# Optimization experiments

Hardware: AMD Instinct MI355X
Metric: run time of the kernel (lower is better)

## Reference

```python
import jax, jax.numpy as jnp
import numpy as np
from jax import lax

B, H, W = 8, 500, 500
M = 2048          # per-image cap on active bottleneck voxels (ragged -> fixed)
GRID = 125        # bottleneck grid size
ENC_RANGE = 125.0
HEADS, ATTN_CH, CH = 4, 128, 64
EPS = 1e-5
NEG = -1e9

def _conv(x, w, b, stride, pad):
    y = lax.conv_general_dilated(x, w, (stride, stride), pad,
                                 dimension_numbers=('NCHW', 'HWIO', 'NCHW'))
    return y + b[None, :, None, None]

def _maxpool2(m):
    return lax.reduce_window(m, -jnp.inf, lax.max, (1, 1, 2, 2), (1, 1, 2, 2), 'VALID')

def setup_inputs():
    key = jax.random.key(0)
    ks = jax.random.split(key, 12)
    occ = (jax.random.uniform(ks[0], (B, 1, H, W)) < 0.005).astype(jnp.float32)
    x = jax.random.normal(ks[1], (B, 1, H, W), dtype=jnp.float32) * occ
    def rn(k, shape, scale):
        return jax.random.normal(k, shape, dtype=jnp.float32) * scale
    return {
        'x': x,
        'w0': rn(ks[2], (3, 3, 1, 32), 0.3), 'b0': jnp.zeros(32, jnp.float32),
        'g0': jnp.ones(32, jnp.float32), 'be0': jnp.zeros(32, jnp.float32),
        'w1': rn(ks[3], (2, 2, 32, 64), 0.1), 'b1': jnp.zeros(64, jnp.float32),
        'g1': jnp.ones(64, jnp.float32), 'be1': jnp.zeros(64, jnp.float32),
        'w2': rn(ks[4], (2, 2, 64, 64), 0.08), 'b2': jnp.zeros(64, jnp.float32),
        'g2': jnp.ones(64, jnp.float32), 'be2': jnp.zeros(64, jnp.float32),
        'wpe': rn(ks[5], (2, 2, CH), 0.5), 'bpe': jnp.zeros((2, CH), jnp.float32),
        'wq': rn(ks[6], (2, CH, ATTN_CH), 0.12), 'bq': jnp.zeros((2, ATTN_CH), jnp.float32),
        'wk': rn(ks[7], (2, CH, ATTN_CH), 0.12), 'bk': jnp.zeros((2, ATTN_CH), jnp.float32),
        'wv': rn(ks[8], (2, CH, ATTN_CH), 0.12), 'bv': jnp.zeros((2, ATTN_CH), jnp.float32),
        'wo': rn(ks[9], (2, ATTN_CH, CH), 0.09), 'bo': jnp.zeros((2, CH), jnp.float32),
        'wh': rn(ks[10], (CH, 4), 0.12), 'bh': jnp.zeros(4, jnp.float32),
    }

def reference(x, w0, b0, g0, be0, w1, b1, g1, be1, w2, b2, g2, be2,
              wpe, bpe, wq, bq, wk, bk, wv, bv, wo, bo, wh, bh):
    # active-site mask (Voxels.from_dense)
    mask0 = (x != 0).any(axis=1, keepdims=True).astype(x.dtype)   # [B,1,500,500]

    def bn_relu(y, g, be):
        # eval-mode BatchNorm1d over active voxel features (running stats 0/1)
        return jax.nn.relu(g[None, :, None, None] * y / jnp.sqrt(1.0 + EPS)
                           + be[None, :, None, None])

    # enc0: submanifold 3x3/s1 -> active set unchanged; inactive inputs are zero
    y = bn_relu(_conv(x, w0, b0, 1, 'SAME'), g0, be0) * mask0
    # enc1/enc2: strided 2x2/s2 -> output active iff any input in window active
    mask1 = _maxpool2(mask0)
    y = bn_relu(_conv(y, w1, b1, 2, 'VALID'), g1, be1) * mask1
    mask2 = _maxpool2(mask1)
    y = bn_relu(_conv(y, w2, b2, 2, 'VALID'), g2, be2) * mask2    # [B,64,125,125]

    # gather active bottleneck voxels per image (ragged -> fixed M + validity mask)
    mflat = mask2.reshape(B, GRID * GRID)
    vals, idx = lax.top_k(mflat, M)     # active-first; stable tie-break (lowest idx)
    valid = vals                        # [B,M] in {0,1}
    feats = jnp.take_along_axis(
        y.reshape(B, CH, GRID * GRID).transpose(0, 2, 1),
        idx[:, :, None], axis=1)        # [B,M,64]
    pos = jnp.stack([idx // GRID, idx % GRID], axis=-1).astype(x.dtype) / ENC_RANGE

    dh = ATTN_CH // HEADS
    kmask = (1.0 - valid)[:, None, None, :] * NEG
    for i in range(2):  # N_ATTN structurally distinct layers
        pe = pos @ wpe[i] + bpe[i]
        h = feats + pe
        q = (h @ wq[i] + bq[i]).reshape(B, M, HEADS, dh)
        k = (h @ wk[i] + bk[i]).reshape(B, M, HEADS, dh)
        v = (h @ wv[i] + bv[i]).reshape(B, M, HEADS, dh)
        s = jnp.einsum('bqhd,bkhd->bhqk', q, k) / jnp.sqrt(jnp.asarray(dh, x.dtype))
        a = jax.nn.softmax(s + kmask, axis=-1)
        o = jnp.einsum('bhqk,bkhd->bqhd', a, v).reshape(B, M, ATTN_CH)
        feats = (feats + o @ wo[i] + bo[i]) * valid[..., None]

    # sparse_global_avg_pool: mean over active voxels per image
    counts = jnp.clip(valid.sum(axis=1, keepdims=True), 1.0, None)
    pooled = feats.sum(axis=1) / counts                            # [B,64]
    return pooled @ wh + bh                                        # [B,4]
```

## Files before the change

kernel.cpp:

```cpp
#include <hip/hip_runtime.h>

#define BDIM   8
#define NPIX   250000
#define G1N    62500
#define G2N    15625
#define NB0    977
#define NB1    245
#define NB2    62
#define CAP0   4096
#define CAP1   4096
#define CAPM   2048
#define CH     64
#define ACH    128
#define NHEADS 4
#define DH     32
#define KSPLIT 4

static constexpr float BN_INV    = 0.99999500003749969f;
static constexpr float ATT_SCALE = 0.17677669529663687f;

typedef _Float16 f16x8 __attribute__((ext_vector_type(8)));
typedef float f32x4 __attribute__((ext_vector_type(4)));

static constexpr size_t E_MAP0  = 0;
static constexpr size_t E_MAP1  = E_MAP0 + (size_t)BDIM*NPIX;
static constexpr size_t E_CNT   = E_MAP1 + (size_t)BDIM*G1N;
static constexpr size_t E_ZEND  = E_CNT + 32;
static constexpr size_t E_BC    = E_ZEND;
static constexpr size_t E_BO    = E_BC + (size_t)3*BDIM*1024;
static constexpr size_t E_BM    = E_BO + (size_t)3*BDIM*1024;
static constexpr size_t E_LIST0 = E_BM + (size_t)3*BDIM*1024*8;
static constexpr size_t E_LIST1 = E_LIST0 + (size_t)BDIM*CAP0;
static constexpr size_t E_LIST2 = E_LIST1 + (size_t)BDIM*CAP1;
static constexpr size_t E_Y0    = E_LIST2 + (size_t)BDIM*CAPM;
static constexpr size_t E_Y1    = E_Y0 + (size_t)BDIM*CAP0*32;
static constexpr size_t E_FE    = E_Y1 + (size_t)BDIM*CAP1*64;
static constexpr size_t E_QF    = E_FE + (size_t)BDIM*CAPM*64;
static constexpr size_t E_KF    = E_QF + (size_t)32*CAPM*32/2;
static constexpr size_t E_VT    = E_KF + (size_t)32*CAPM*32/2;
static constexpr size_t E_O     = E_VT + (size_t)32*CAPM*32/2;


__device__ __forceinline__ bool act0(const float* x, int pix, int b) {
  return (pix < NPIX) && (x[(size_t)b * NPIX + pix] != 0.f);
}
__device__ __forceinline__ bool act1(const int* map0, int p, int b) {
  if (p >= G1N) return false;
  int i = p / 250, j = p - i * 250;
  const int* m = map0 + (size_t)b * NPIX + (2 * i) * 500 + 2 * j;
  return (m[0] | m[1] | m[500] | m[501]) != 0;
}
__device__ __forceinline__ bool act2(const int* map1, int p, int b) {
  if (p >= G2N) return false;
  int i = p / 125, j = p - i * 125;
  const int* m = map1 + (size_t)b * G1N + (2 * i) * 250 + 2 * j;
  return (m[0] | m[1] | m[250] | m[251]) != 0;
}

#define COUNT_BODY(ACT_EXPR)                                            \
  int idx = blockIdx.x * 256 + threadIdx.x;                             \
  int b = blockIdx.y;                                                   \
  bool act = (ACT_EXPR);                                                \
  unsigned long long mask = __ballot(act);                              \
  __shared__ int wc[4];                                                 \
  if ((threadIdx.x & 63) == 0) {                                        \
    wc[threadIdx.x >> 6] = __popcll(mask);                              \
    bm[((size_t)b * 1024 + blockIdx.x) * 4 + (threadIdx.x >> 6)] = mask;\
  }                                                                     \
  __syncthreads();                                                      \
  if (threadIdx.x == 0)                                                 \
    bcnt[b * 1024 + blockIdx.x] = wc[0] + wc[1] + wc[2] + wc[3];

__global__ void k_cnt0(const float* __restrict__ x, int* __restrict__ bcnt,
                       unsigned long long* __restrict__ bm) {
  COUNT_BODY(act0(x, idx, b))
}
__global__ void k_cnt1(const int* __restrict__ map0, int* __restrict__ bcnt,
                       unsigned long long* __restrict__ bm) {
  COUNT_BODY(act1(map0, idx, b))
}
__global__ void k_cnt2(const int* __restrict__ map1, int* __restrict__ bcnt,
                       unsigned long long* __restrict__ bm) {
  COUNT_BODY(act2(map1, idx, b))
}

__global__ __launch_bounds__(256) void k_scan(const int* __restrict__ bcnt,
                                              int* __restrict__ boff,
                                              int* __restrict__ cnt,
                                              int nblk, int cbase) {
  int b = blockIdx.x;
  int t = threadIdx.x;
  int base = t * 4;
  int v[4];
  int ts = 0;
#pragma unroll
  for (int u = 0; u < 4; ++u) {
    v[u] = (base + u < nblk) ? bcnt[b * 1024 + base + u] : 0;
    ts += v[u];
  }
  int lane = t & 63, w = t >> 6;
  int incl = ts;
#pragma unroll
  for (int off = 1; off < 64; off <<= 1) {
    int o = __shfl_up(incl, off, 64);
    if (lane >= off) incl += o;
  }
  __shared__ int wsum[4];
  if (lane == 63) wsum[w] = incl;
  __syncthreads();
  int woff = 0;
#pragma unroll
  for (int k = 0; k < 3; ++k) if (k < w) woff += wsum[k];
  int run = woff + incl - ts;
#pragma unroll
  for (int u = 0; u < 4; ++u) {
    if (base + u < nblk) boff[b * 1024 + base + u] = run;
    run += v[u];
  }
  if (t == 255) cnt[cbase + b] = run;
}

#define EMIT_PROLOG                                                     \
  int idx = blockIdx.x * 256 + threadIdx.x;                             \
  int b = blockIdx.y;                                                   \
  int lane = threadIdx.x & 63;                                          \
  unsigned long long mask =                                             \
      bm[((size_t)b * 1024 + blockIdx.x) * 4 + (threadIdx.x >> 6)];     \
  bool act = (mask >> lane) & 1;                                        \
  __shared__ int wbase[4];                                              \
  if (lane == 0) wbase[threadIdx.x >> 6] = __popcll(mask);              \
  __syncthreads();                                                      \
  if (threadIdx.x == 0) {                                               \
    int s = boff[b * 1024 + blockIdx.x];                                \
    for (int w = 0; w < 4; ++w) { int c = wbase[w]; wbase[w] = s; s += c; } \
  }                                                                     \
  __syncthreads();                                                      \
  int slot = wbase[threadIdx.x >> 6] + __popcll(mask & ((1ull << lane) - 1ull));

__global__ void k_emit0(const unsigned long long* __restrict__ bm,
                        const int* __restrict__ boff,
                        int* __restrict__ map0, int* __restrict__ list0) {
  EMIT_PROLOG
  if (act && slot < CAP0) {
    list0[b * CAP0 + slot] = idx;
    map0[(size_t)b * NPIX + idx] = slot + 1;
  }
}
__global__ void k_emit1(const unsigned long long* __restrict__ bm,
                        const int* __restrict__ boff,
                        int* __restrict__ map1, int* __restrict__ list1) {
  EMIT_PROLOG
  if (act && slot < CAP1) {
    list1[b * CAP1 + slot] = idx;
    map1[(size_t)b * G1N + idx] = slot + 1;
  }
}
__global__ void k_emit2(const unsigned long long* __restrict__ bm,
                        const int* __restrict__ boff,
                        int* __restrict__ list2) {
  EMIT_PROLOG
  if (act && slot < CAPM) list2[b * CAPM + slot] = idx;
}


__global__ void k_y0(const float* __restrict__ x, const float* __restrict__ w0,
                     const float* __restrict__ b0, const float* __restrict__ g0,
                     const float* __restrict__ be0,
                     const int* __restrict__ list0, const int* __restrict__ cnt,
                     float* __restrict__ y0) {
  int t = blockIdx.x * 256 + threadIdx.x;
  int b = t >> 17;
  int r = t & 131071;
  int slot = r >> 5, c = r & 31;
  int n = min(cnt[b], CAP0);
  if (slot >= n) return;
  int pix = list0[b * CAP0 + slot];
  int i = pix / 500, j = pix - i * 500;
  float acc = b0[c];
#pragma unroll
  for (int di = 0; di < 3; ++di) {
    int ii = i + di - 1;
    if ((unsigned)ii >= 500u) continue;
#pragma unroll
    for (int dj = 0; dj < 3; ++dj) {
      int jj = j + dj - 1;
      if ((unsigned)jj >= 500u) continue;
      acc += x[(size_t)b * NPIX + ii * 500 + jj] * w0[(di * 3 + dj) * 32 + c];
    }
  }
  float o = g0[c] * acc * BN_INV + be0[c];
  y0[((size_t)(b * CAP0) + slot) * 32 + c] = fmaxf(o, 0.f);
}

__global__ __launch_bounds__(256) void k_y1(
    const float* __restrict__ y0, const float* __restrict__ w1,
    const float* __restrict__ b1, const float* __restrict__ g1,
    const float* __restrict__ be1,
    const int* __restrict__ map0, const int* __restrict__ list1,
    const int* __restrict__ cnt, float* __restrict__ y1) {
  int b = blockIdx.x & 7;
  int qblk = blockIdx.x >> 3;
  int sub = threadIdx.x >> 6;
  int co = threadIdx.x & 63;
  int n = min(cnt[BDIM + b], CAP1);
  if (qblk * 32 >= n) return;
  int s0 = qblk * 32 + sub * 8;
  __shared__ float inT[4][4][32][8];
  for (int idx = co; idx < 1024; idx += 64) {
    int s = idx & 7;
    int r = idx >> 3;
    int ci = r & 31, pp = r >> 5;
    float v = 0.f;
    int sg = s0 + s;
    if (sg < n) {
      int p = list1[b * CAP1 + sg];
      int i = p / 250, j = p - i * 250;
      int sm = map0[(size_t)b * NPIX + (2 * i + (pp >> 1)) * 500 + (2 * j + (pp & 1))];
      if (sm) v = y0[((size_t)(b * CAP0) + (sm - 1)) * 32 + ci];
    }
    inT[sub][pp][ci][s] = v;
  }
  __syncthreads();
  float acc[8];
#pragma unroll
  for (int s = 0; s < 8; ++s) acc[s] = b1[co];
#pragma unroll 2
  for (int pp = 0; pp < 4; ++pp)
    for (int ci = 0; ci < 32; ++ci) {
      float wv = w1[((pp << 5) + ci) * 64 + co];
      float4 i0 = *(const float4*)&inT[sub][pp][ci][0];
      float4 i1 = *(const float4*)&inT[sub][pp][ci][4];
      acc[0] += i0.x * wv; acc[1] += i0.y * wv; acc[2] += i0.z * wv; acc[3] += i0.w * wv;
      acc[4] += i1.x * wv; acc[5] += i1.y * wv; acc[6] += i1.z * wv; acc[7] += i1.w * wv;
    }
  int smax = min(8, n - s0);
  for (int s = 0; s < smax; ++s) {
    float o = g1[co] * acc[s] * BN_INV + be1[co];
    y1[((size_t)(b * CAP1) + s0 + s) * 64 + co] = fmaxf(o, 0.f);
  }
}

__global__ __launch_bounds__(256) void k_y2(
    const float* __restrict__ y1, const float* __restrict__ w2,
    const float* __restrict__ b2, const float* __restrict__ g2,
    const float* __restrict__ be2,
    const int* __restrict__ map1, const int* __restrict__ list2,
    const int* __restrict__ cnt, float* __restrict__ feats) {
  int b = blockIdx.x & 7;
  int qblk = blockIdx.x >> 3;
  int sub = threadIdx.x >> 6;
  int co = threadIdx.x & 63;
  int n = min(cnt[2 * BDIM + b], CAPM);
  if (qblk * 32 >= n) return;
  int s0 = qblk * 32 + sub * 8;
  __shared__ float inT[4][4][64][8];
  for (int idx = co; idx < 2048; idx += 64) {
    int s = idx & 7;
    int r = idx >> 3;
    int ci = r & 63, pp = r >> 6;
    float v = 0.f;
    int sg = s0 + s;
    if (sg < n) {
      int p = list2[b * CAPM + sg];
      int i = p / 125, j = p - i * 125;
      int sm = map1[(size_t)b * G1N + (2 * i + (pp >> 1)) * 250 + (2 * j + (pp & 1))];
      if (sm) v = y1[((size_t)(b * CAP1) + (sm - 1)) * 64 + ci];
    }
    inT[sub][pp][ci][s] = v;
  }
  __syncthreads();
  float acc[8];
#pragma unroll
  for (int s = 0; s < 8; ++s) acc[s] = b2[co];
#pragma unroll 2
  for (int pp = 0; pp < 4; ++pp)
    for (int ci = 0; ci < 64; ++ci) {
      float wv = w2[((pp << 6) + ci) * 64 + co];
      float4 i0 = *(const float4*)&inT[sub][pp][ci][0];
      float4 i1 = *(const float4*)&inT[sub][pp][ci][4];
      acc[0] += i0.x * wv; acc[1] += i0.y * wv; acc[2] += i0.z * wv; acc[3] += i0.w * wv;
      acc[4] += i1.x * wv; acc[5] += i1.y * wv; acc[6] += i1.z * wv; acc[7] += i1.w * wv;
    }
  int smax = min(8, n - s0);
  for (int s = 0; s < smax; ++s) {
    float o = g2[co] * acc[s] * BN_INV + be2[co];
    feats[((size_t)(b * CAPM) + s0 + s) * 64 + co] = fmaxf(o, 0.f);
  }
}


__global__ __launch_bounds__(256) void k_qkv(
    const float* __restrict__ feats, const int* __restrict__ list2,
    const int* __restrict__ cnt,
    const float* __restrict__ wpe, const float* __restrict__ bpe,
    const float* __restrict__ wq, const float* __restrict__ bq,
    const float* __restrict__ wk, const float* __restrict__ bk,
    const float* __restrict__ wv, const float* __restrict__ bv,
    int layer, _Float16* __restrict__ qf, _Float16* __restrict__ kf,
    _Float16* __restrict__ vt) {
  int b = blockIdx.x & 7;
  int qblk = blockIdx.x >> 3;
  int sub = threadIdx.x >> 7;
  int o = threadIdx.x & 127;
  int n = min(cnt[2 * BDIM + b], CAPM);
  if (qblk * 16 >= n) return;
  int s0 = qblk * 16 + sub * 8;
  __shared__ float hT[2][64][8];
  for (int idx = o; idx < 512; idx += 128) {
    int s = idx & 7, c = idx >> 3;
    float hv = 0.f;
    int sg = s0 + s;
    if (sg < n) {
      int p = list2[b * CAPM + sg];
      int i = p / 125, j = p - i * 125;
      hv = feats[((size_t)(b * CAPM) + sg) * 64 + c]
         + (float)i * (1.f / 125.f) * wpe[(layer * 2 + 0) * 64 + c]
         + (float)j * (1.f / 125.f) * wpe[(layer * 2 + 1) * 64 + c]
         + bpe[layer * 64 + c];
    }
    hT[sub][c][s] = hv;
  }
  __syncthreads();
  float accq[8], acck[8], accv[8];
  float bqv = bq[layer * 128 + o], bkv = bk[layer * 128 + o], bvv = bv[layer * 128 + o];
#pragma unroll
  for (int s = 0; s < 8; ++s) { accq[s] = bqv; acck[s] = bkv; accv[s] = bvv; }
  const float* wq_ = wq + (size_t)layer * 64 * 128 + o;
  const float* wk_ = wk + (size_t)layer * 64 * 128 + o;
  const float* wv_ = wv + (size_t)layer * 64 * 128 + o;
  for (int c = 0; c < 64; ++c) {
    float wqv = wq_[c * 128], wkv = wk_[c * 128], wvv = wv_[c * 128];
    float4 h0 = *(const float4*)&hT[sub][c][0];
    float4 h1 = *(const float4*)&hT[sub][c][4];
    float hh[8] = {h0.x, h0.y, h0.z, h0.w, h1.x, h1.y, h1.z, h1.w};
#pragma unroll
    for (int s = 0; s < 8; ++s) {
      accq[s] += hh[s] * wqv; acck[s] += hh[s] * wkv; accv[s] += hh[s] * wvv;
    }
  }
  int hd = o >> 5, d = o & 31;
  size_t bh = (size_t)(b * NHEADS + hd);
  int smax = min(8, n - s0);
  for (int s = 0; s < smax; ++s) {
    size_t rb = (bh * CAPM + s0 + s) * 32 + d;
    qf[rb] = (_Float16)accq[s];
    kf[rb] = (_Float16)acck[s];
    vt[(bh * 32 + d) * CAPM + s0 + s] = (_Float16)accv[s];
  }
}


union U4H8 { uint4 u; f16x8 h; };
union PKU  { _Float16 h[2]; unsigned int u; };

#define LOADK(K0, K1, K2, K3, T0)                                          \
  K0 = *(const f16x8*)(kf + (bh + (T0) + qr) * 32 + g8);                   \
  K1 = *(const f16x8*)(kf + (bh + (T0) + 16 + qr) * 32 + g8);              \
  K2 = *(const f16x8*)(kf + (bh + (T0) + 32 + qr) * 32 + g8);              \
  K3 = *(const f16x8*)(kf + (bh + (T0) + 48 + qr) * 32 + g8);

#define LOADV(V0, V1, V2, V3, T0)                                          \
  V0 = *(const f16x8*)(vbase + (size_t)qr * CAPM + (T0) + g8);             \
  V1 = *(const f16x8*)(vbase + (size_t)(16 + qr) * CAPM + (T0) + g8);      \
  V2 = *(const f16x8*)(vbase + (size_t)qr * CAPM + (T0) + 32 + g8);        \
  V3 = *(const f16x8*)(vbase + (size_t)(16 + qr) * CAPM + (T0) + 32 + g8);

#define PROCESS(K0, K1, K2, K3, V0, V1, V2, V3, T0)                        \
  {                                                                        \
    f32x4 z = {0.f, 0.f, 0.f, 0.f};                                        \
    f32x4 st0 = __builtin_amdgcn_mfma_f32_16x16x32_f16(K0, fq, z, 0, 0, 0);\
    f32x4 st1 = __builtin_amdgcn_mfma_f32_16x16x32_f16(K1, fq, z, 0, 0, 0);\
    f32x4 st2 = __builtin_amdgcn_mfma_f32_16x16x32_f16(K2, fq, z, 0, 0, 0);\
    f32x4 st3 = __builtin_amdgcn_mfma_f32_16x16x32_f16(K3, fq, z, 0, 0, 0);\
    if ((T0) + 64 > n) {                                                   \
      _Pragma("unroll") for (int r = 0; r < 4; ++r) {                      \
        if ((T0) + 4 * g + r >= n)      st0[r] = -1e30f;                   \
        if ((T0) + 16 + 4 * g + r >= n) st1[r] = -1e30f;                   \
        if ((T0) + 32 + 4 * g + r >= n) st2[r] = -1e30f;                   \
        if ((T0) + 48 + 4 * g + r >= n) st3[r] = -1e30f;                   \
      }                                                                    \
    }                                                                      \
    float tm = st0[0];                                                     \
    _Pragma("unroll") for (int r = 1; r < 4; ++r) tm = fmaxf(tm, st0[r]);  \
    _Pragma("unroll") for (int r = 0; r < 4; ++r) tm = fmaxf(tm, st1[r]);  \
    _Pragma("unroll") for (int r = 0; r < 4; ++r) tm = fmaxf(tm, st2[r]);  \
    _Pragma("unroll") for (int r = 0; r < 4; ++r) tm = fmaxf(tm, st3[r]);  \
    tm = fmaxf(tm, __shfl_xor(tm, 16));                                    \
    tm = fmaxf(tm, __shfl_xor(tm, 32));                                    \
    float mn = fmaxf(m, tm * ATT_SCALE);                                   \
    float f_ = __expf(m - mn);                                             \
    m = mn;                                                                \
    float ls = 0.f;                                                        \
    {                                                                      \
      PKU a, c;                                                            \
      a.h[0] = (_Float16)__expf(st0[0] * ATT_SCALE - mn);                  \
      a.h[1] = (_Float16)__expf(st0[1] * ATT_SCALE - mn);                  \
      c.h[0] = (_Float16)__expf(st0[2] * ATT_SCALE - mn);                  \
      c.h[1] = (_Float16)__expf(st0[3] * ATT_SCALE - mn);                  \
      ls += (float)a.h[0] + (float)a.h[1] + (float)c.h[0] + (float)c.h[1]; \
      P[(qr * 32 + 0 + 2 * g) ^ swz] = a.u;                                \
      P[(qr * 32 + 1 + 2 * g) ^ swz] = c.u;                                \
      a.h[0] = (_Float16)__expf(st1[0] * ATT_SCALE - mn);                  \
      a.h[1] = (_Float16)__expf(st1[1] * ATT_SCALE - mn);                  \
      c.h[0] = (_Float16)__expf(st1[2] * ATT_SCALE - mn);                  \
      c.h[1] = (_Float16)__expf(st1[3] * ATT_SCALE - mn);                  \
      ls += (float)a.h[0] + (float)a.h[1] + (float)c.h[0] + (float)c.h[1]; \
      P[(qr * 32 + 8 + 2 * g) ^ swz] = a.u;                                \
      P[(qr * 32 + 9 + 2 * g) ^ swz] = c.u;                                \
      a.h[0] = (_Float16)__expf(st2[0] * ATT_SCALE - mn);                  \
      a.h[1] = (_Float16)__expf(st2[1] * ATT_SCALE - mn);                  \
      c.h[0] = (_Float16)__expf(st2[2] * ATT_SCALE - mn);                  \
      c.h[1] = (_Float16)__expf(st2[3] * ATT_SCALE - mn);                  \
      ls += (float)a.h[0] + (float)a.h[1] + (float)c.h[0] + (float)c.h[1]; \
      P[(qr * 32 + 16 + 2 * g) ^ swz] = a.u;                               \
      P[(qr * 32 + 17 + 2 * g) ^ swz] = c.u;                               \
      a.h[0] = (_Float16)__expf(st3[0] * ATT_SCALE - mn);                  \
      a.h[1] = (_Float16)__expf(st3[1] * ATT_SCALE - mn);                  \
      c.h[0] = (_Float16)__expf(st3[2] * ATT_SCALE - mn);                  \
      c.h[1] = (_Float16)__expf(st3[3] * ATT_SCALE - mn);                  \
      ls += (float)a.h[0] + (float)a.h[1] + (float)c.h[0] + (float)c.h[1]; \
      P[(qr * 32 + 24 + 2 * g) ^ swz] = a.u;                               \
      P[(qr * 32 + 25 + 2 * g) ^ swz] = c.u;                               \
    }                                                                      \
    l = l * f_ + ls;                                                       \
    __builtin_amdgcn_sched_barrier(0);                                     \
    U4H8 pa0, pa1;                                                         \
    pa0.u = *(const uint4*)&P[(qr * 32 + 4 * g) ^ swz];                    \
    pa1.u = *(const uint4*)&P[(qr * 32 + 16 + 4 * g) ^ swz];               \
    acc0[0] *= f_; acc0[1] *= f_; acc0[2] *= f_; acc0[3] *= f_;            \
    acc1[0] *= f_; acc1[1] *= f_; acc1[2] *= f_; acc1[3] *= f_;            \
    acc0 = __builtin_amdgcn_mfma_f32_16x16x32_f16(V0, pa0.h, acc0, 0, 0, 0);\
    acc1 = __builtin_amdgcn_mfma_f32_16x16x32_f16(V1, pa0.h, acc1, 0, 0, 0);\
    acc0 = __builtin_amdgcn_mfma_f32_16x16x32_f16(V2, pa1.h, acc0, 0, 0, 0);\
    acc1 = __builtin_amdgcn_mfma_f32_16x16x32_f16(V3, pa1.h, acc1, 0, 0, 0);\
  }

__global__ __launch_bounds__(256) void k_attn(
    const _Float16* __restrict__ qf, const _Float16* __restrict__ kf,
    const _Float16* __restrict__ vt, const int* __restrict__ cnt,
    _Float16* __restrict__ obuf) {
  int b  = blockIdx.x & 7;
  int rr = blockIdx.x >> 3;
  int qt = rr & 127;
  int h  = rr >> 7;
  int n = min(cnt[2 * BDIM + b], CAPM);
  int q0 = qt * 16;
  if (q0 >= n) return;
  int ks = threadIdx.x >> 6;
  int lane = threadIdx.x & 63;
  int g = lane >> 4, qr = lane & 15;
  int g8 = g * 8;
  size_t bh = (size_t)(b * NHEADS + h) * CAPM;
  const _Float16* vbase = vt + (size_t)(b * NHEADS + h) * 32 * CAPM;
  f16x8 fq = *(const f16x8*)(qf + (bh + q0 + qr) * 32 + g8);
  f32x4 acc0 = {0.f, 0.f, 0.f, 0.f}, acc1 = {0.f, 0.f, 0.f, 0.f};
  float m = -1e30f, l = 0.f;
  __shared__ unsigned int P4[4][512];
  __shared__ float partA[4][16][33];
  __shared__ float mlA[4][16][2];
  unsigned int* P = P4[ks];
  int swz = (qr & 7) << 2;

  int nt = (n + 63) >> 6;
  int tpc = (nt + KSPLIT - 1) / KSPLIT;
  int tb = ks * tpc, te = min(nt, tb + tpc);
  if (tb < te) {
    f16x8 ka0, ka1, ka2, ka3, va0, va1, va2, va3;
    f16x8 kb0, kb1, kb2, kb3, vb0, vb1, vb2, vb3;
    LOADK(ka0, ka1, ka2, ka3, tb * 64)
    LOADV(va0, va1, va2, va3, tb * 64)
    for (int t = tb; t < te; t += 2) {
      if (t + 1 < te) {
        LOADK(kb0, kb1, kb2, kb3, (t + 1) * 64)
        LOADV(vb0, vb1, vb2, vb3, (t + 1) * 64)
      }
      PROCESS(ka0, ka1, ka2, ka3, va0, va1, va2, va3, t * 64)
      if (t + 1 < te) {
        if (t + 2 < te) {
          LOADK(ka0, ka1, ka2, ka3, (t + 2) * 64)
          LOADV(va0, va1, va2, va3, (t + 2) * 64)
        }
        PROCESS(kb0, kb1, kb2, kb3, vb0, vb1, vb2, vb3, (t + 1) * 64)
      }
    }
  }
  l += __shfl_xor(l, 16);
  l += __shfl_xor(l, 32);
#pragma unroll
  for (int r = 0; r < 4; ++r) {
    partA[ks][qr][4 * g + r] = acc0[r];
    partA[ks][qr][16 + 4 * g + r] = acc1[r];
  }
  if (g == 0) { mlA[ks][qr][0] = m; mlA[ks][qr][1] = l; }
  __syncthreads();
  int t = threadIdx.x;
  int s = t >> 4;
  int c0 = (t & 15) * 2;
  int tok = q0 + s;
  if (tok < n) {
    float m0 = mlA[0][s][0], l0 = mlA[0][s][1];
    float m1 = mlA[1][s][0], l1 = mlA[1][s][1];
    float m2 = mlA[2][s][0], l2 = mlA[2][s][1];
    float m3 = mlA[3][s][0], l3 = mlA[3][s][1];
    float M = fmaxf(fmaxf(m0, m1), fmaxf(m2, m3));
    float w0_ = __expf(m0 - M), w1_ = __expf(m1 - M);
    float w2_ = __expf(m2 - M), w3_ = __expf(m3 - M);
    float invL = 1.f / (w0_ * l0 + w1_ * l1 + w2_ * l2 + w3_ * l3);
    float v0 = (partA[0][s][c0] * w0_ + partA[1][s][c0] * w1_ +
                partA[2][s][c0] * w2_ + partA[3][s][c0] * w3_) * invL;
    float v1 = (partA[0][s][c0 + 1] * w0_ + partA[1][s][c0 + 1] * w1_ +
                partA[2][s][c0 + 1] * w2_ + partA[3][s][c0 + 1] * w3_) * invL;
    _Float16* op = obuf + ((size_t)b * CAPM + tok) * ACH + h * DH;
    op[c0] = (_Float16)v0;
    op[c0 + 1] = (_Float16)v1;
  }
}


__global__ __launch_bounds__(256) void k_proj(
    const _Float16* __restrict__ obuf, const float* __restrict__ wo,
    const float* __restrict__ bo, const int* __restrict__ cnt,
    int layer, float* __restrict__ feats) {
  int b = blockIdx.x & 7;
  int sblk = blockIdx.x >> 3;
  int s0 = sblk * 4;
  int n = min(cnt[2 * BDIM + b], CAPM);
  if (s0 >= n) return;
  __shared__ float oT[128][4];
  int t = threadIdx.x;
#pragma unroll
  for (int k = 0; k < 2; ++k) {
    int id = t + k * 256;
    int c = id >> 2, s = id & 3;
    int sg = s0 + s;
    oT[c][s] = (sg < n) ? (float)obuf[((size_t)b * CAPM + sg) * ACH + c] : 0.f;
  }
  __syncthreads();
  int s = t >> 6, co = t & 63;
  float acc = bo[layer * 64 + co];
  const float* w = wo + (size_t)layer * 128 * 64 + co;
#pragma unroll 8
  for (int c = 0; c < 128; ++c) acc += oT[c][s] * w[c * 64];
  int tok = s0 + s;
  if (tok < n) feats[((size_t)(b * CAPM) + tok) * 64 + co] += acc;
}


__global__ __launch_bounds__(1024) void k_head(
    const float* __restrict__ feats, const float* __restrict__ wh,
    const float* __restrict__ bhd, const int* __restrict__ cnt,
    float* __restrict__ out) {
  int b = blockIdx.x;
  int n = min(cnt[2 * BDIM + b], CAPM);
  int c = threadIdx.x & 63, chunk = threadIdx.x >> 6;
  int lo = chunk * 128, hi = min(n, lo + 128);
  float s = 0.f;
  for (int mm = lo; mm < hi; ++mm)
    s += feats[((size_t)(b * CAPM) + mm) * 64 + c];
  __shared__ float red[16][64];
  __shared__ float pooled[64];
  red[chunk][c] = s;
  __syncthreads();
  if (threadIdx.x < 64) {
    float tot = 0.f;
#pragma unroll
    for (int k = 0; k < 16; ++k) tot += red[k][c];
    pooled[c] = tot / (float)max(n, 1);
  }
  __syncthreads();
  if (threadIdx.x < 4) {
    float o = bhd[threadIdx.x];
#pragma unroll
    for (int c2 = 0; c2 < 64; ++c2) o += pooled[c2] * wh[c2 * 4 + threadIdx.x];
    out[b * 4 + threadIdx.x] = o;
  }
}


extern "C" void kernel_launch(void* const* d_in, const int* in_sizes, int n_in,
                              void* d_out, int out_size, void* d_ws, size_t ws_size,
                              hipStream_t stream) {
  const float* x   = (const float*)d_in[0];
  const float* w0  = (const float*)d_in[1];
  const float* b0  = (const float*)d_in[2];
  const float* g0  = (const float*)d_in[3];
  const float* be0 = (const float*)d_in[4];
  const float* w1  = (const float*)d_in[5];
  const float* b1  = (const float*)d_in[6];
  const float* g1  = (const float*)d_in[7];
  const float* be1 = (const float*)d_in[8];
  const float* w2  = (const float*)d_in[9];
  const float* b2  = (const float*)d_in[10];
  const float* g2  = (const float*)d_in[11];
  const float* be2 = (const float*)d_in[12];
  const float* wpe = (const float*)d_in[13];
  const float* bpe = (const float*)d_in[14];
  const float* wq  = (const float*)d_in[15];
  const float* bq  = (const float*)d_in[16];
  const float* wk  = (const float*)d_in[17];
  const float* bk  = (const float*)d_in[18];
  const float* wv  = (const float*)d_in[19];
  const float* bv  = (const float*)d_in[20];
  const float* wo  = (const float*)d_in[21];
  const float* bo  = (const float*)d_in[22];
  const float* wh  = (const float*)d_in[23];
  const float* bh  = (const float*)d_in[24];

  int* wsI = (int*)d_ws;
  float* wsF = (float*)d_ws;
  unsigned long long* bm = (unsigned long long*)(wsI + E_BM);
  _Float16* qf = (_Float16*)(wsI + E_QF);
  _Float16* kf = (_Float16*)(wsI + E_KF);
  _Float16* vt = (_Float16*)(wsI + E_VT);
  _Float16* ob = (_Float16*)(wsI + E_O);

  hipMemsetAsync(d_ws, 0, E_ZEND * 4, stream);

  k_cnt0<<<dim3(NB0, BDIM), 256, 0, stream>>>(x, wsI + E_BC + 0 * BDIM * 1024,
                                              bm + 0 * BDIM * 4096);
  k_scan<<<BDIM, 256, 0, stream>>>(wsI + E_BC + 0 * BDIM * 1024,
                                   wsI + E_BO + 0 * BDIM * 1024,
                                   wsI + E_CNT, NB0, 0);
  k_emit0<<<dim3(NB0, BDIM), 256, 0, stream>>>(bm + 0 * BDIM * 4096,
                                               wsI + E_BO + 0 * BDIM * 1024,
                                               wsI + E_MAP0, wsI + E_LIST0);
  k_y0<<<(BDIM * CAP0 * 32) / 256, 256, 0, stream>>>(
      x, w0, b0, g0, be0, wsI + E_LIST0, wsI + E_CNT, wsF + E_Y0);
  k_cnt1<<<dim3(NB1, BDIM), 256, 0, stream>>>(wsI + E_MAP0,
                                              wsI + E_BC + 1 * BDIM * 1024,
                                              bm + 1 * BDIM * 4096);
  k_scan<<<BDIM, 256, 0, stream>>>(wsI + E_BC + 1 * BDIM * 1024,
                                   wsI + E_BO + 1 * BDIM * 1024,
                                   wsI + E_CNT, NB1, BDIM);
  k_emit1<<<dim3(NB1, BDIM), 256, 0, stream>>>(bm + 1 * BDIM * 4096,
                                               wsI + E_BO + 1 * BDIM * 1024,
                                               wsI + E_MAP1, wsI + E_LIST1);
  k_y1<<<BDIM * (CAP1 / 32), 256, 0, stream>>>(
      wsF + E_Y0, w1, b1, g1, be1, wsI + E_MAP0, wsI + E_LIST1, wsI + E_CNT, wsF + E_Y1);
  k_cnt2<<<dim3(NB2, BDIM), 256, 0, stream>>>(wsI + E_MAP1,
                                              wsI + E_BC + 2 * BDIM * 1024,
                                              bm + 2 * BDIM * 4096);
  k_scan<<<BDIM, 256, 0, stream>>>(wsI + E_BC + 2 * BDIM * 1024,
                                   wsI + E_BO + 2 * BDIM * 1024,
                                   wsI + E_CNT, NB2, 2 * BDIM);
  k_emit2<<<dim3(NB2, BDIM), 256, 0, stream>>>(bm + 2 * BDIM * 4096,
                                               wsI + E_BO + 2 * BDIM * 1024,
                                               wsI + E_LIST2);
  k_y2<<<BDIM * (CAPM / 32), 256, 0, stream>>>(
      wsF + E_Y1, w2, b2, g2, be2, wsI + E_MAP1, wsI + E_LIST2, wsI + E_CNT, wsF + E_FE);

  for (int layer = 0; layer < 2; ++layer) {
    k_qkv<<<BDIM * (CAPM / 16), 256, 0, stream>>>(
        wsF + E_FE, wsI + E_LIST2, wsI + E_CNT, wpe, bpe, wq, bq, wk, bk, wv, bv,
        layer, qf, kf, vt);
    k_attn<<<BDIM * NHEADS * (CAPM / 16), 256, 0, stream>>>(
        qf, kf, vt, wsI + E_CNT, ob);
    k_proj<<<BDIM * (CAPM / 4), 256, 0, stream>>>(
        ob, wo, bo, wsI + E_CNT, layer, wsF + E_FE);
  }

  k_head<<<BDIM, 1024, 0, stream>>>(wsF + E_FE, wh, bh, wsI + E_CNT, (float*)d_out);
}
```

Before: 246.7 us.

## Split attention softmax into two independent streams and fold scale into Q

Folds the softmax scale and log2(e) into Q when it is written, so the inner loop can use exp2 without per-element multiplies. Alternating key tiles now keep separate running max/sum/accumulator state and separate P buffers in shared memory, which removes the serial dependency between consecutive tiles and allows their work to interleave. The two streams are merged at the end, and the sched_barrier is dropped. It also adds a launch-bounds occupancy hint, at the cost of more registers and twice the shared memory for P.

Result: slower. 325.4 us (+31.9%).

```diff
diff --git a/kernel.cpp b/kernel.cpp
--- a/kernel.cpp
+++ b/kernel.cpp
@@ -16,8 +16,8 @@
 #define DH     32
 #define KSPLIT 4
 
-static constexpr float BN_INV    = 0.99999500003749969f;
-static constexpr float ATT_SCALE = 0.17677669529663687f;
+static constexpr float BN_INV = 0.99999500003749969f;
+static constexpr float SCALE2 = 0.25505654734044769f;
 
 typedef _Float16 f16x8 __attribute__((ext_vector_type(8)));
 typedef float f32x4 __attribute__((ext_vector_type(4)));
@@ -343,7 +343,7 @@
   int smax = min(8, n - s0);
   for (int s = 0; s < smax; ++s) {
     size_t rb = (bh * CAPM + s0 + s) * 32 + d;
-    qf[rb] = (_Float16)accq[s];
+    qf[rb] = (_Float16)(accq[s] * SCALE2);
     kf[rb] = (_Float16)acck[s];
     vt[(bh * 32 + d) * CAPM + s0 + s] = (_Float16)accv[s];
   }
@@ -365,7 +365,7 @@
   V2 = *(const f16x8*)(vbase + (size_t)qr * CAPM + (T0) + 32 + g8);        \
   V3 = *(const f16x8*)(vbase + (size_t)(16 + qr) * CAPM + (T0) + 32 + g8);
 
-#define PROCESS(K0, K1, K2, K3, V0, V1, V2, V3, T0)                        \
+#define PROCESS(SM, SL, A0, A1, PB, K0, K1, K2, K3, V0, V1, V2, V3, T0)    \
   {                                                                        \
     f32x4 z = {0.f, 0.f, 0.f, 0.f};                                        \
     f32x4 st0 = __builtin_amdgcn_mfma_f32_16x16x32_f16(K0, fq, z, 0, 0, 0);\
@@ -387,55 +387,54 @@
     _Pragma("unroll") for (int r = 0; r < 4; ++r) tm = fmaxf(tm, st3[r]);  \
     tm = fmaxf(tm, __shfl_xor(tm, 16));                                    \
     tm = fmaxf(tm, __shfl_xor(tm, 32));                                    \
-    float mn = fmaxf(m, tm * ATT_SCALE);                                   \
-    float f_ = __expf(m - mn);                                             \
-    m = mn;                                                                \
+    float mn = fmaxf(SM, tm);                                              \
+    float f_ = exp2f(SM - mn);                                             \
+    SM = mn;                                                               \
     float ls = 0.f;                                                        \
     {                                                                      \
       PKU a, c;                                                            \
-      a.h[0] = (_Float16)__expf(st0[0] * ATT_SCALE - mn);                  \
-      a.h[1] = (_Float16)__expf(st0[1] * ATT_SCALE - mn);                  \
-      c.h[0] = (_Float16)__expf(st0[2] * ATT_SCALE - mn);                  \
-      c.h[1] = (_Float16)__expf(st0[3] * ATT_SCALE - mn);                  \
+      a.h[0] = (_Float16)exp2f(st0[0] - mn);                               \
+      a.h[1] = (_Float16)exp2f(st0[1] - mn);                               \
+      c.h[0] = (_Float16)exp2f(st0[2] - mn);                               \
+      c.h[1] = (_Float16)exp2f(st0[3] - mn);                               \
       ls += (float)a.h[0] + (float)a.h[1] + (float)c.h[0] + (float)c.h[1]; \
-      P[(qr * 32 + 0 + 2 * g) ^ swz] = a.u;                                \
-      P[(qr * 32 + 1 + 2 * g) ^ swz] = c.u;                                \
-      a.h[0] = (_Float16)__expf(st1[0] * ATT_SCALE - mn);                  \
-      a.h[1] = (_Float16)__expf(st1[1] * ATT_SCALE - mn);                  \
-      c.h[0] = (_Float16)__expf(st1[2] * ATT_SCALE - mn);                  \
-      c.h[1] = (_Float16)__expf(st1[3] * ATT_SCALE - mn);                  \
+      PB[(qr * 32 + 0 + 2 * g) ^ swz] = a.u;                               \
+      PB[(qr * 32 + 1 + 2 * g) ^ swz] = c.u;                               \
+      a.h[0] = (_Float16)exp2f(st1[0] - mn);                               \
+      a.h[1] = (_Float16)exp2f(st1[1] - mn);                               \
+      c.h[0] = (_Float16)exp2f(st1[2] - mn);                               \
+      c.h[1] = (_Float16)exp2f(st1[3] - mn);                               \
       ls += (float)a.h[0] + (float)a.h[1] + (float)c.h[0] + (float)c.h[1]; \
-      P[(qr * 32 + 8 + 2 * g) ^ swz] = a.u;                                \
-      P[(qr * 32 + 9 + 2 * g) ^ swz] = c.u;                                \
-      a.h[0] = (_Float16)__expf(st2[0] * ATT_SCALE - mn);                  \
-      a.h[1] = (_Float16)__expf(st2[1] * ATT_SCALE - mn);                  \
-      c.h[0] = (_Float16)__expf(st2[2] * ATT_SCALE - mn);                  \
-      c.h[1] = (_Float16)__expf(st2[3] * ATT_SCALE - mn);                  \
+      PB[(qr * 32 + 8 + 2 * g) ^ swz] = a.u;                               \
+      PB[(qr * 32 + 9 + 2 * g) ^ swz] = c.u;                               \
+      a.h[0] = (_Float16)exp2f(st2[0] - mn);                               \
+      a.h[1] = (_Float16)exp2f(st2[1] - mn);                               \
+      c.h[0] = (_Float16)exp2f(st2[2] - mn);                               \
+      c.h[1] = (_Float16)exp2f(st2[3] - mn);                               \
       ls += (float)a.h[0] + (float)a.h[1] + (float)c.h[0] + (float)c.h[1]; \
-      P[(qr * 32 + 16 + 2 * g) ^ swz] = a.u;                               \
-      P[(qr * 32 + 17 + 2 * g) ^ swz] = c.u;                               \
-      a.h[0] = (_Float16)__expf(st3[0] * ATT_SCALE - mn);                  \
-      a.h[1] = (_Float16)__expf(st3[1] * ATT_SCALE - mn);                  \
-      c.h[0] = (_Float16)__expf(st3[2] * ATT_SCALE - mn);                  \
-      c.h[1] = (_Float16)__expf(st3[3] * ATT_SCALE - mn);                  \
+      PB[(qr * 32 + 16 + 2 * g) ^ swz] = a.u;                              \
+      PB[(qr * 32 + 17 + 2 * g) ^ swz] = c.u;                              \
+      a.h[0] = (_Float16)exp2f(st3[0] - mn);                               \
+      a.h[1] = (_Float16)exp2f(st3[1] - mn);                               \
+      c.h[0] = (_Float16)exp2f(st3[2] - mn);                               \
+      c.h[1] = (_Float16)exp2f(st3[3] - mn);                               \
       ls += (float)a.h[0] + (float)a.h[1] + (float)c.h[0] + (float)c.h[1]; \
-      P[(qr * 32 + 24 + 2 * g) ^ swz] = a.u;                               \
-      P[(qr * 32 + 25 + 2 * g) ^ swz] = c.u;                               \
+      PB[(qr * 32 + 24 + 2 * g) ^ swz] = a.u;                              \
+      PB[(qr * 32 + 25 + 2 * g) ^ swz] = c.u;                              \
     }                                                                      \
-    l = l * f_ + ls;                                                       \
-    __builtin_amdgcn_sched_barrier(0);                                     \
+    SL = SL * f_ + ls;                                                     \
     U4H8 pa0, pa1;                                                         \
-    pa0.u = *(const uint4*)&P[(qr * 32 + 4 * g) ^ swz];                    \
-    pa1.u = *(const uint4*)&P[(qr * 32 + 16 + 4 * g) ^ swz];               \
-    acc0[0] *= f_; acc0[1] *= f_; acc0[2] *= f_; acc0[3] *= f_;            \
-    acc1[0] *= f_; acc1[1] *= f_; acc1[2] *= f_; acc1[3] *= f_;            \
-    acc0 = __builtin_amdgcn_mfma_f32_16x16x32_f16(V0, pa0.h, acc0, 0, 0, 0);\
-    acc1 = __builtin_amdgcn_mfma_f32_16x16x32_f16(V1, pa0.h, acc1, 0, 0, 0);\
-    acc0 = __builtin_amdgcn_mfma_f32_16x16x32_f16(V2, pa1.h, acc0, 0, 0, 0);\
-    acc1 = __builtin_amdgcn_mfma_f32_16x16x32_f16(V3, pa1.h, acc1, 0, 0, 0);\
-  }
-
-__global__ __launch_bounds__(256) void k_attn(
+    pa0.u = *(const uint4*)&PB[(qr * 32 + 4 * g) ^ swz];                   \
+    pa1.u = *(const uint4*)&PB[(qr * 32 + 16 + 4 * g) ^ swz];              \
+    A0[0] *= f_; A0[1] *= f_; A0[2] *= f_; A0[3] *= f_;                    \
+    A1[0] *= f_; A1[1] *= f_; A1[2] *= f_; A1[3] *= f_;                    \
+    A0 = __builtin_amdgcn_mfma_f32_16x16x32_f16(V0, pa0.h, A0, 0, 0, 0);   \
+    A1 = __builtin_amdgcn_mfma_f32_16x16x32_f16(V1, pa0.h, A1, 0, 0, 0);   \
+    A0 = __builtin_amdgcn_mfma_f32_16x16x32_f16(V2, pa1.h, A0, 0, 0, 0);   \
+    A1 = __builtin_amdgcn_mfma_f32_16x16x32_f16(V3, pa1.h, A1, 0, 0, 0);   \
+  }
+
+__global__ __launch_bounds__(256, 4) void k_attn(
     const _Float16* __restrict__ qf, const _Float16* __restrict__ kf,
     const _Float16* __restrict__ vt, const int* __restrict__ cnt,
     _Float16* __restrict__ obuf) {
@@ -453,12 +452,14 @@
   size_t bh = (size_t)(b * NHEADS + h) * CAPM;
   const _Float16* vbase = vt + (size_t)(b * NHEADS + h) * 32 * CAPM;
   f16x8 fq = *(const f16x8*)(qf + (bh + q0 + qr) * 32 + g8);
-  f32x4 acc0 = {0.f, 0.f, 0.f, 0.f}, acc1 = {0.f, 0.f, 0.f, 0.f};
-  float m = -1e30f, l = 0.f;
-  __shared__ unsigned int P4[4][512];
+  f32x4 aA0 = {0.f, 0.f, 0.f, 0.f}, aA1 = {0.f, 0.f, 0.f, 0.f};
+  f32x4 aB0 = {0.f, 0.f, 0.f, 0.f}, aB1 = {0.f, 0.f, 0.f, 0.f};
+  float mA = -1e30f, lA = 0.f, mB = -1e30f, lB = 0.f;
+  __shared__ unsigned int P4[8][512];
   __shared__ float partA[4][16][33];
   __shared__ float mlA[4][16][2];
-  unsigned int* P = P4[ks];
+  unsigned int* PA = P4[2 * ks];
+  unsigned int* PB = P4[2 * ks + 1];
   int swz = (qr & 7) << 2;
 
   int nt = (n + 63) >> 6;
@@ -474,24 +475,33 @@
         LOADK(kb0, kb1, kb2, kb3, (t + 1) * 64)
         LOADV(vb0, vb1, vb2, vb3, (t + 1) * 64)
       }
-      PROCESS(ka0, ka1, ka2, ka3, va0, va1, va2, va3, t * 64)
+      PROCESS(mA, lA, aA0, aA1, PA, ka0, ka1, ka2, ka3, va0, va1, va2, va3, t * 64)
       if (t + 1 < te) {
         if (t + 2 < te) {
           LOADK(ka0, ka1, ka2, ka3, (t + 2) * 64)
           LOADV(va0, va1, va2, va3, (t + 2) * 64)
         }
-        PROCESS(kb0, kb1, kb2, kb3, vb0, vb1, vb2, vb3, (t + 1) * 64)
+        PROCESS(mB, lB, aB0, aB1, PB, kb0, kb1, kb2, kb3, vb0, vb1, vb2, vb3, (t + 1) * 64)
       }
     }
-  }
-  l += __shfl_xor(l, 16);
-  l += __shfl_xor(l, 32);
+    float mw = fmaxf(mA, mB);
+    float wa = exp2f(mA - mw), wb = exp2f(mB - mw);
+    lA = lA * wa + lB * wb;
+#pragma unroll
+    for (int r = 0; r < 4; ++r) {
+      aA0[r] = aA0[r] * wa + aB0[r] * wb;
+      aA1[r] = aA1[r] * wa + aB1[r] * wb;
+    }
+    mA = mw;
+  }
+  lA += __shfl_xor(lA, 16);
+  lA += __shfl_xor(lA, 32);
 #pragma unroll
   for (int r = 0; r < 4; ++r) {
-    partA[ks][qr][4 * g + r] = acc0[r];
-    partA[ks][qr][16 + 4 * g + r] = acc1[r];
-  }
-  if (g == 0) { mlA[ks][qr][0] = m; mlA[ks][qr][1] = l; }
+    partA[ks][qr][4 * g + r] = aA0[r];
+    partA[ks][qr][16 + 4 * g + r] = aA1[r];
+  }
+  if (g == 0) { mlA[ks][qr][0] = mA; mlA[ks][qr][1] = lA; }
   __syncthreads();
   int t = threadIdx.x;
   int s = t >> 4;
@@ -503,8 +513,8 @@
     float m2 = mlA[2][s][0], l2 = mlA[2][s][1];
     float m3 = mlA[3][s][0], l3 = mlA[3][s][1];
     float M = fmaxf(fmaxf(m0, m1), fmaxf(m2, m3));
-    float w0_ = __expf(m0 - M), w1_ = __expf(m1 - M);
-    float w2_ = __expf(m2 - M), w3_ = __expf(m3 - M);
+    float w0_ = exp2f(m0 - M), w1_ = exp2f(m1 - M);
+    float w2_ = exp2f(m2 - M), w3_ = exp2f(m3 - M);
     float invL = 1.f / (w0_ * l0 + w1_ * l1 + w2_ * l2 + w3_ * l3);
     float v0 = (partA[0][s][c0] * w0_ + partA[1][s][c0] * w1_ +
                 partA[2][s][c0] * w2_ + partA[3][s][c0] * w3_) * invL;
```
